# Kernel optimization log

Measured on AMD Instinct MI355X. Metric: run time of the kernel, lower is better.

Reference implementation:

```python
import jax, jax.numpy as jnp
import numpy as np

B, S, D = 8, 2048, 1024
EPS = 1e-5


def setup_inputs() -> dict:
    key = jax.random.key(0)
    ks = jax.random.split(key, 8)
    s = 1.0 / np.sqrt(D)
    return {
        "x": jax.random.normal(ks[0], (B, S, D), dtype=jnp.float32),
        "Wq": jax.random.normal(ks[1], (D, D), dtype=jnp.float32) * s,
        "bq": jnp.zeros((D,), dtype=jnp.float32),
        "Wk": jax.random.normal(ks[2], (D, D), dtype=jnp.float32) * s,
        "bk": jnp.zeros((D,), dtype=jnp.float32),
        "Wv": jax.random.normal(ks[3], (D, D), dtype=jnp.float32) * s,
        "bv": jnp.zeros((D,), dtype=jnp.float32),
        "gamma": jnp.ones((D,), dtype=jnp.float32),
        "beta": jnp.zeros((D,), dtype=jnp.float32),
    }


def reference(x, Wq, bq, Wk, bk, Wv, bv, gamma, beta):
    # Linear layers (torch convention: y = x @ W^T + b)
    Q = jnp.einsum('bsd,ed->bse', x, Wq) + bq
    K = jnp.einsum('bsd,ed->bse', x, Wk) + bk
    V = jnp.einsum('bsd,ed->bse', x, Wv) + bv
    scale = 1.0 / jnp.sqrt(jnp.asarray(D, dtype=x.dtype))
    scores = jnp.einsum('bqd,bkd->bqk', Q, K) * scale  # [B,S,S]
    attn = jax.nn.softmax(scores, axis=-1)
    out = jnp.einsum('bqk,bkd->bqd', attn, V) + x  # attention + residual
    # LayerNorm over last dim
    mu = jnp.mean(out, axis=-1, keepdims=True)
    var = jnp.var(out, axis=-1, keepdims=True)
    return (out - mu) * jax.lax.rsqrt(var + EPS) * gamma + beta
```

## Files before the change

kernel.cpp:

```cpp
#include <hip/hip_runtime.h>


typedef __bf16 bf16x8 __attribute__((ext_vector_type(8)));
typedef float f32x4 __attribute__((ext_vector_type(4)));

#define BM 128
#define BN 128
#define BK 32

enum { M_QK = 0, M_VT = 1, M_SC = 2, M_PV = 3 };

__device__ __forceinline__ unsigned short f2b(float f) {
  union { float f; unsigned int u; } v; v.f = f;
  return (unsigned short)((v.u + 0x7FFFu + ((v.u >> 16) & 1u)) >> 16);
}

__device__ __forceinline__ void gload_lds16(const void* g, void* l) {
  __builtin_amdgcn_global_load_lds(
      (const __attribute__((address_space(1))) void*)g,
      (__attribute__((address_space(3))) void*)l, 16, 0, 0);
}

template <int MODE>
__global__ __launch_bounds__(256) void gemm_bf16(
    const unsigned short* __restrict__ A, const unsigned short* __restrict__ B,
    void* __restrict__ Cv, const float* __restrict__ aux, float alpha,
    int K, int ldaE, int ldbE, int ldcE,
    size_t sA, size_t sB, size_t sC, size_t sR)
{
  const int t = threadIdx.x, l = t & 63, w = t >> 6;
  const int wm = w >> 1, wn = w & 1;
  const int bz = blockIdx.z;
  A += (size_t)bz * sA;
  B += (size_t)bz * sB;
  const int gm0 = blockIdx.y * BM, gn0 = blockIdx.x * BN;

  __shared__ __align__(16) unsigned short As[BM * BK];
  __shared__ __align__(16) unsigned short Bs[BN * BK];

  f32x4 acc[4][4];
#pragma unroll
  for (int i = 0; i < 4; ++i)
#pragma unroll
    for (int j = 0; j < 4; ++j) acc[i][j] = f32x4{0.f, 0.f, 0.f, 0.f};

  const int srow = w * 16 + (l >> 2);
  const int scolb = (l & 3) << 4;
  const int rr = l & 15;
  const int k0 = (l >> 4) << 3;

  for (int kt = 0; kt < K; kt += BK) {
    __syncthreads();
#pragma unroll
    for (int c = 0; c < 2; ++c) {
      const int r = c * 64 + srow;
      gload_lds16((const char*)(A + (size_t)(gm0 + r) * ldaE + kt) + scolb,
                  (char*)As + c * 4096 + w * 1024);
      gload_lds16((const char*)(B + (size_t)(gn0 + r) * ldbE + kt) + scolb,
                  (char*)Bs + c * 4096 + w * 1024);
    }
    __syncthreads();
    bf16x8 av[4], bv[4];
#pragma unroll
    for (int i = 0; i < 4; ++i)
      av[i] = *(const bf16x8*)&As[(wm * 64 + i * 16 + rr) * BK + k0];
#pragma unroll
    for (int j = 0; j < 4; ++j)
      bv[j] = *(const bf16x8*)&Bs[(wn * 64 + j * 16 + rr) * BK + k0];
#pragma unroll
    for (int i = 0; i < 4; ++i)
#pragma unroll
      for (int j = 0; j < 4; ++j)
        acc[i][j] = __builtin_amdgcn_mfma_f32_16x16x32_bf16(av[i], bv[j], acc[i][j], 0, 0, 0);
  }

  const int col_l = l & 15, row0_l = (l >> 4) << 2;
#pragma unroll
  for (int i = 0; i < 4; ++i) {
    const int gr = gm0 + wm * 64 + i * 16 + row0_l;
#pragma unroll
    for (int j = 0; j < 4; ++j) {
      const int gc = gn0 + wn * 64 + j * 16 + col_l;
      if constexpr (MODE == M_QK) {
        unsigned short* C = (unsigned short*)Cv;
        const float b = aux[gc];
#pragma unroll
        for (int r = 0; r < 4; ++r)
          C[(size_t)(gr + r) * ldcE + gc] = f2b(acc[i][j][r] + b);
      } else if constexpr (MODE == M_VT) {
        unsigned short* C = (unsigned short*)Cv;
        const float b = aux[gc];
        const int bat = gr >> 11, lm = gr & 2047;
        ushort4 o = make_ushort4(f2b(acc[i][j][0] + b), f2b(acc[i][j][1] + b),
                                 f2b(acc[i][j][2] + b), f2b(acc[i][j][3] + b));
        *(ushort4*)&C[(size_t)bat * sC + (size_t)gc * ldcE + lm] = o;
      } else if constexpr (MODE == M_SC) {
        float* C = (float*)Cv + (size_t)bz * sC;
        float* p = C + (size_t)gr * ldcE + gc;
#pragma unroll
        for (int r = 0; r < 4; ++r) p[(size_t)r * ldcE] = acc[i][j][r] * alpha;
      } else {
        float* C = (float*)Cv + (size_t)bz * sC;
        const float* R = aux + (size_t)bz * sR;
        float* p = C + (size_t)gr * ldcE + gc;
        const float* q = R + (size_t)gr * ldcE + gc;
#pragma unroll
        for (int r = 0; r < 4; ++r) p[(size_t)r * ldcE] = acc[i][j][r] + q[(size_t)r * ldcE];
      }
    }
  }
}

__global__ __launch_bounds__(256) void f32_to_bf16(
    const float* __restrict__ s, unsigned short* __restrict__ d)
{
  const size_t i = (size_t)blockIdx.x * 256 + threadIdx.x;
  const float4 a = ((const float4*)s)[i * 2];
  const float4 b = ((const float4*)s)[i * 2 + 1];
  ((ushort4*)d)[i * 2]     = make_ushort4(f2b(a.x), f2b(a.y), f2b(a.z), f2b(a.w));
  ((ushort4*)d)[i * 2 + 1] = make_ushort4(f2b(b.x), f2b(b.y), f2b(b.z), f2b(b.w));
}

__global__ __launch_bounds__(256) void softmax2048_bf16(float* __restrict__ S)
{
  __shared__ float redm[4];
  __shared__ float reds[4];
  const int t = threadIdx.x;
  float* p = S + (size_t)blockIdx.x * 2048;
  float4 a = *(const float4*)&p[t * 4];
  float4 b = *(const float4*)&p[t * 4 + 1024];
  float m = fmaxf(fmaxf(fmaxf(a.x, a.y), fmaxf(a.z, a.w)),
                  fmaxf(fmaxf(b.x, b.y), fmaxf(b.z, b.w)));
#pragma unroll
  for (int o = 32; o; o >>= 1) m = fmaxf(m, __shfl_xor(m, o));
  if ((t & 63) == 0) redm[t >> 6] = m;
  __syncthreads();
  m = fmaxf(fmaxf(redm[0], redm[1]), fmaxf(redm[2], redm[3]));
  a.x = __expf(a.x - m); a.y = __expf(a.y - m);
  a.z = __expf(a.z - m); a.w = __expf(a.w - m);
  b.x = __expf(b.x - m); b.y = __expf(b.y - m);
  b.z = __expf(b.z - m); b.w = __expf(b.w - m);
  float s = a.x + a.y + a.z + a.w + b.x + b.y + b.z + b.w;
#pragma unroll
  for (int o = 32; o; o >>= 1) s += __shfl_xor(s, o);
  if ((t & 63) == 0) reds[t >> 6] = s;
  __syncthreads();
  s = reds[0] + reds[1] + reds[2] + reds[3];
  const float inv = 1.0f / s;
  unsigned short* pb = (unsigned short*)p;
  *(ushort4*)&pb[t * 4] =
      make_ushort4(f2b(a.x * inv), f2b(a.y * inv), f2b(a.z * inv), f2b(a.w * inv));
  *(ushort4*)&pb[1024 + t * 4] =
      make_ushort4(f2b(b.x * inv), f2b(b.y * inv), f2b(b.z * inv), f2b(b.w * inv));
}

__global__ __launch_bounds__(64) void ln1024(
    float* __restrict__ O, const float* __restrict__ g, const float* __restrict__ be)
{
  const int l = threadIdx.x;
  float* p = O + (size_t)blockIdx.x * 1024;
  float4 v[4];
#pragma unroll
  for (int i = 0; i < 4; ++i) v[i] = *(const float4*)&p[l * 4 + i * 256];
  float s = 0.f, q = 0.f;
#pragma unroll
  for (int i = 0; i < 4; ++i) {
    s += v[i].x + v[i].y + v[i].z + v[i].w;
    q += v[i].x * v[i].x + v[i].y * v[i].y + v[i].z * v[i].z + v[i].w * v[i].w;
  }
#pragma unroll
  for (int o = 32; o; o >>= 1) { s += __shfl_xor(s, o); q += __shfl_xor(q, o); }
  const float mu = s * (1.0f / 1024.0f);
  const float var = q * (1.0f / 1024.0f) - mu * mu;
  const float rs = rsqrtf(var + 1e-5f);
#pragma unroll
  for (int i = 0; i < 4; ++i) {
    const float4 gg = *(const float4*)&g[l * 4 + i * 256];
    const float4 bb = *(const float4*)&be[l * 4 + i * 256];
    float4 o4;
    o4.x = (v[i].x - mu) * rs * gg.x + bb.x;
    o4.y = (v[i].y - mu) * rs * gg.y + bb.y;
    o4.z = (v[i].z - mu) * rs * gg.z + bb.z;
    o4.w = (v[i].w - mu) * rs * gg.w + bb.w;
    *(float4*)&p[l * 4 + i * 256] = o4;
  }
}

extern "C" void kernel_launch(void* const* d_in, const int* in_sizes, int n_in,
                              void* d_out, int out_size, void* d_ws, size_t ws_size,
                              hipStream_t stream) {
  (void)in_sizes; (void)n_in; (void)out_size; (void)ws_size;
  constexpr int Bb = 8, S = 2048, D = 1024;
  const size_t BS = (size_t)Bb * S;
  const size_t ND = BS * (size_t)D;

  const float* x     = (const float*)d_in[0];
  const float* Wq    = (const float*)d_in[1];
  const float* bq    = (const float*)d_in[2];
  const float* Wk    = (const float*)d_in[3];
  const float* bk    = (const float*)d_in[4];
  const float* Wv    = (const float*)d_in[5];
  const float* bv    = (const float*)d_in[6];
  const float* gamma = (const float*)d_in[7];
  const float* beta  = (const float*)d_in[8];
  float* out = (float*)d_out;

  unsigned short* xb = (unsigned short*)d_ws;
  unsigned short* Qb = xb + ND;
  unsigned short* Kb = Qb + ND;
  unsigned short* Vt = Kb + ND;
  float* Sbuf = (float*)(Vt + ND);
  unsigned short* Wqb = (unsigned short*)Sbuf;
  unsigned short* Wkb = Wqb + (size_t)D * D;
  unsigned short* Wvb = Wkb + (size_t)D * D;

  f32_to_bf16<<<dim3(8192), dim3(256), 0, stream>>>(x, xb);
  f32_to_bf16<<<dim3(512), dim3(256), 0, stream>>>(Wq, Wqb);
  f32_to_bf16<<<dim3(512), dim3(256), 0, stream>>>(Wk, Wkb);
  f32_to_bf16<<<dim3(512), dim3(256), 0, stream>>>(Wv, Wvb);

  const dim3 blk(256);
  const dim3 g1(D / BN, (int)(BS / BM), 1);
  gemm_bf16<M_QK><<<g1, blk, 0, stream>>>(xb, Wqb, Qb, bq, 1.f, D, D, D, D, 0, 0, 0, 0);
  gemm_bf16<M_QK><<<g1, blk, 0, stream>>>(xb, Wkb, Kb, bk, 1.f, D, D, D, D, 0, 0, 0, 0);
  gemm_bf16<M_VT><<<g1, blk, 0, stream>>>(xb, Wvb, Vt, bv, 1.f, D, D, D, S, 0, 0,
                                          (size_t)D * S, 0);
  const dim3 g2(S / BN, S / BM, Bb);
  gemm_bf16<M_SC><<<g2, blk, 0, stream>>>(Qb, Kb, Sbuf, nullptr, 0.03125f, D, D, D, S,
                                          (size_t)S * D, (size_t)S * D, (size_t)S * S, 0);
  softmax2048_bf16<<<dim3((int)BS), blk, 0, stream>>>(Sbuf);
  const dim3 g3(D / BN, S / BM, Bb);
  gemm_bf16<M_PV><<<g3, blk, 0, stream>>>(
      (const unsigned short*)Sbuf, Vt, out, x, 1.f, S, 2 * S, S, D,
      (size_t)S * 2 * S, (size_t)D * S, (size_t)S * D, (size_t)S * D);
  ln1024<<<dim3((int)BS), dim3(64), 0, stream>>>(out, gamma, beta);
}
```

Before: 613.9 us.

## Replace GEMMs with 256x256 double-buffered swizzled kernel and fuse QKV projection

```diff
diff --git a/kernel.cpp b/kernel.cpp
--- a/kernel.cpp
+++ b/kernel.cpp
@@ -4,108 +4,184 @@
 typedef __bf16 bf16x8 __attribute__((ext_vector_type(8)));
 typedef float f32x4 __attribute__((ext_vector_type(4)));
 
-#define BM 128
-#define BN 128
-#define BK 32
-
-enum { M_QK = 0, M_VT = 1, M_SC = 2, M_PV = 3 };
+enum { M_QKV = 0, M_SC = 1, M_PV = 2 };
 
 __device__ __forceinline__ unsigned short f2b(float f) {
   union { float f; unsigned int u; } v; v.f = f;
   return (unsigned short)((v.u + 0x7FFFu + ((v.u >> 16) & 1u)) >> 16);
 }
 
-__device__ __forceinline__ void gload_lds16(const void* g, void* l) {
-  __builtin_amdgcn_global_load_lds(
-      (const __attribute__((address_space(1))) void*)g,
-      (__attribute__((address_space(3))) void*)l, 16, 0, 0);
+#define GL16(gsrc, ldst)                                         \
+  __builtin_amdgcn_global_load_lds(                              \
+      (const __attribute__((address_space(1))) void*)(gsrc),     \
+      (__attribute__((address_space(3))) void*)(ldst), 16, 0, 0)
+
+__device__ __forceinline__ void stage_tile(
+    const unsigned short* Ab, const unsigned short* Bb, char* lds,
+    int b, int tau, int gm0, int gn0, int ldaE, int ldbE, int t)
+{
+  const int kc = tau << 6;
+  const int row4 = t >> 3;
+  const int c = (t & 7) << 4;
+  const int wb = (t & ~63) * 16;
+#pragma unroll
+  for (int r = 0; r < 4; ++r) {
+    const int row = r * 64 + row4;
+    const int cs = c ^ ((row & 12) << 3);
+    GL16((const char*)(Ab + (size_t)(gm0 + row) * ldaE + kc) + cs,
+         lds + b * 65536 + r * 8192 + wb);
+    __builtin_amdgcn_sched_barrier(0);
+  }
+#pragma unroll
+  for (int r = 0; r < 4; ++r) {
+    const int row = r * 64 + row4;
+    const int cs = c ^ ((row & 12) << 3);
+    GL16((const char*)(Bb + (size_t)(gn0 + row) * ldbE + kc) + cs,
+         lds + b * 65536 + 32768 + r * 8192 + wb);
+    __builtin_amdgcn_sched_barrier(0);
+  }
+}
+
+__device__ __forceinline__ bf16x8 ldsrd(const char* lds, int base, int row, int kb) {
+  int p = row * 128 + kb;
+  p ^= (p & 0x600) >> 4;
+  return *(const bf16x8*)(lds + base + p);
 }
 
 template <int MODE>
-__global__ __launch_bounds__(256) void gemm_bf16(
+__global__ __launch_bounds__(512, 2) void gemm8(
     const unsigned short* __restrict__ A, const unsigned short* __restrict__ B,
-    void* __restrict__ Cv, const float* __restrict__ aux, float alpha,
-    int K, int ldaE, int ldbE, int ldcE,
-    size_t sA, size_t sB, size_t sC, size_t sR)
-{
+    void* __restrict__ C0, void* __restrict__ C1, void* __restrict__ C2,
+    const float* __restrict__ x0, const float* __restrict__ x1,
+    const float* __restrict__ x2,
+    int K, int ldaE, int ldbE, size_t sA, size_t sB)
+{
+  extern __shared__ char lds[];
   const int t = threadIdx.x, l = t & 63, w = t >> 6;
-  const int wm = w >> 1, wn = w & 1;
   const int bz = blockIdx.z;
-  A += (size_t)bz * sA;
-  B += (size_t)bz * sB;
-  const int gm0 = blockIdx.y * BM, gn0 = blockIdx.x * BN;
-
-  __shared__ __align__(16) unsigned short As[BM * BK];
-  __shared__ __align__(16) unsigned short Bs[BN * BK];
-
-  f32x4 acc[4][4];
-#pragma unroll
-  for (int i = 0; i < 4; ++i)
-#pragma unroll
-    for (int j = 0; j < 4; ++j) acc[i][j] = f32x4{0.f, 0.f, 0.f, 0.f};
-
-  const int srow = w * 16 + (l >> 2);
-  const int scolb = (l & 3) << 4;
-  const int rr = l & 15;
-  const int k0 = (l >> 4) << 3;
-
-  for (int kt = 0; kt < K; kt += BK) {
-    __syncthreads();
-#pragma unroll
-    for (int c = 0; c < 2; ++c) {
-      const int r = c * 64 + srow;
-      gload_lds16((const char*)(A + (size_t)(gm0 + r) * ldaE + kt) + scolb,
-                  (char*)As + c * 4096 + w * 1024);
-      gload_lds16((const char*)(B + (size_t)(gn0 + r) * ldbE + kt) + scolb,
-                  (char*)Bs + c * 4096 + w * 1024);
+  const unsigned short* Ab = A + (size_t)bz * sA;
+  const unsigned short* Bb = B + (size_t)bz * sB;
+  const int gm0 = blockIdx.y * 256, gn0 = blockIdx.x * 256;
+  const int lo16 = l & 15, hi4 = l >> 4;
+  const int kb0 = hi4 * 16;
+  const int nt = K >> 6;
+
+  f32x4 acc[2][16];
+#pragma unroll
+  for (int i = 0; i < 2; ++i)
+#pragma unroll
+    for (int j = 0; j < 16; ++j) acc[i][j] = f32x4{0.f, 0.f, 0.f, 0.f};
+
+  stage_tile(Ab, Bb, lds, 0, 0, gm0, gn0, ldaE, ldbE, t);
+
+  bf16x8 af[2][2];
+  for (int tau = 0; tau < nt; ++tau) {
+    const int abase = (tau & 1) * 65536, bbase = abase + 32768;
+    const bool more = (tau + 1) < nt;
+    asm volatile("s_waitcnt vmcnt(3)" ::: "memory");
+    __builtin_amdgcn_sched_barrier(0);
+    __builtin_amdgcn_s_barrier();
+    __builtin_amdgcn_sched_barrier(0);
+    if (more)
+      stage_tile(Ab, Bb, lds, (tau & 1) ^ 1, tau + 1, gm0, gn0, ldaE, ldbE, t);
+    bf16x8 bf[4][2];
+#pragma unroll
+    for (int mf = 0; mf < 2; ++mf)
+#pragma unroll
+      for (int ks = 0; ks < 2; ++ks)
+        af[mf][ks] = ldsrd(lds, abase, w * 32 + mf * 16 + lo16, ks * 64 + kb0);
+#pragma unroll
+    for (int nf = 0; nf < 4; ++nf)
+#pragma unroll
+      for (int ks = 0; ks < 2; ++ks)
+        bf[nf][ks] = ldsrd(lds, bbase, nf * 16 + lo16, ks * 64 + kb0);
+    asm volatile("s_waitcnt lgkmcnt(0)" ::: "memory");
+    __builtin_amdgcn_sched_barrier(0);
+    __builtin_amdgcn_s_setprio(1);
+#pragma unroll
+    for (int mf = 0; mf < 2; ++mf)
+#pragma unroll
+      for (int nf = 0; nf < 4; ++nf)
+#pragma unroll
+        for (int ks = 0; ks < 2; ++ks)
+          acc[mf][nf] = __builtin_amdgcn_mfma_f32_16x16x32_bf16(
+              af[mf][ks], bf[nf][ks], acc[mf][nf], 0, 0, 0);
+    __builtin_amdgcn_s_setprio(0);
+#pragma unroll
+    for (int p = 1; p < 4; ++p) {
+      if (p == 1) {
+        if (more) asm volatile("s_waitcnt vmcnt(10)" ::: "memory");
+        else      asm volatile("s_waitcnt vmcnt(2)" ::: "memory");
+      } else if (p == 2) {
+        if (more) asm volatile("s_waitcnt vmcnt(9)" ::: "memory");
+        else      asm volatile("s_waitcnt vmcnt(1)" ::: "memory");
+      } else {
+        if (more) asm volatile("s_waitcnt vmcnt(8)" ::: "memory");
+        else      asm volatile("s_waitcnt vmcnt(0)" ::: "memory");
+      }
+      __builtin_amdgcn_sched_barrier(0);
+      __builtin_amdgcn_s_barrier();
+      __builtin_amdgcn_sched_barrier(0);
+#pragma unroll
+      for (int nf = 0; nf < 4; ++nf)
+#pragma unroll
+        for (int ks = 0; ks < 2; ++ks)
+          bf[nf][ks] = ldsrd(lds, bbase, (p * 4 + nf) * 16 + lo16, ks * 64 + kb0);
+      asm volatile("s_waitcnt lgkmcnt(0)" ::: "memory");
+      __builtin_amdgcn_sched_barrier(0);
+      __builtin_amdgcn_s_setprio(1);
+#pragma unroll
+      for (int mf = 0; mf < 2; ++mf)
+#pragma unroll
+        for (int nf = 0; nf < 4; ++nf)
+#pragma unroll
+          for (int ks = 0; ks < 2; ++ks)
+            acc[mf][p * 4 + nf] = __builtin_amdgcn_mfma_f32_16x16x32_bf16(
+                af[mf][ks], bf[nf][ks], acc[mf][p * 4 + nf], 0, 0, 0);
+      __builtin_amdgcn_s_setprio(0);
     }
-    __syncthreads();
-    bf16x8 av[4], bv[4];
-#pragma unroll
-    for (int i = 0; i < 4; ++i)
-      av[i] = *(const bf16x8*)&As[(wm * 64 + i * 16 + rr) * BK + k0];
-#pragma unroll
-    for (int j = 0; j < 4; ++j)
-      bv[j] = *(const bf16x8*)&Bs[(wn * 64 + j * 16 + rr) * BK + k0];
-#pragma unroll
-    for (int i = 0; i < 4; ++i)
-#pragma unroll
-      for (int j = 0; j < 4; ++j)
-        acc[i][j] = __builtin_amdgcn_mfma_f32_16x16x32_bf16(av[i], bv[j], acc[i][j], 0, 0, 0);
-  }
-
-  const int col_l = l & 15, row0_l = (l >> 4) << 2;
-#pragma unroll
-  for (int i = 0; i < 4; ++i) {
-    const int gr = gm0 + wm * 64 + i * 16 + row0_l;
-#pragma unroll
-    for (int j = 0; j < 4; ++j) {
-      const int gc = gn0 + wn * 64 + j * 16 + col_l;
-      if constexpr (MODE == M_QK) {
-        unsigned short* C = (unsigned short*)Cv;
-        const float b = aux[gc];
-#pragma unroll
-        for (int r = 0; r < 4; ++r)
-          C[(size_t)(gr + r) * ldcE + gc] = f2b(acc[i][j][r] + b);
-      } else if constexpr (MODE == M_VT) {
-        unsigned short* C = (unsigned short*)Cv;
-        const float b = aux[gc];
-        const int bat = gr >> 11, lm = gr & 2047;
-        ushort4 o = make_ushort4(f2b(acc[i][j][0] + b), f2b(acc[i][j][1] + b),
-                                 f2b(acc[i][j][2] + b), f2b(acc[i][j][3] + b));
-        *(ushort4*)&C[(size_t)bat * sC + (size_t)gc * ldcE + lm] = o;
+  }
+
+#pragma unroll
+  for (int mf = 0; mf < 2; ++mf) {
+    const int grow = gm0 + w * 32 + mf * 16 + hi4 * 4;
+#pragma unroll
+    for (int nf = 0; nf < 16; ++nf) {
+      const int gc = gn0 + nf * 16 + lo16;
+      if constexpr (MODE == M_QKV) {
+        if (gc < 1024) {
+          unsigned short* Q = (unsigned short*)C0;
+          const float b = x0[gc];
+#pragma unroll
+          for (int r = 0; r < 4; ++r)
+            Q[(size_t)(grow + r) * 1024 + gc] = f2b(acc[mf][nf][r] + b);
+        } else if (gc < 2048) {
+          unsigned short* Kk = (unsigned short*)C1;
+          const float b = x1[gc - 1024];
+#pragma unroll
+          for (int r = 0; r < 4; ++r)
+            Kk[(size_t)(grow + r) * 1024 + (gc - 1024)] = f2b(acc[mf][nf][r] + b);
+        } else {
+          unsigned short* Vt = (unsigned short*)C2;
+          const float b = x2[gc - 2048];
+          const int bat = grow >> 11, lm = grow & 2047;
+          ushort4 o = make_ushort4(
+              f2b(acc[mf][nf][0] + b), f2b(acc[mf][nf][1] + b),
+              f2b(acc[mf][nf][2] + b), f2b(acc[mf][nf][3] + b));
+          *(ushort4*)&Vt[(size_t)bat * 2097152 + (size_t)(gc - 2048) * 2048 + lm] = o;
+        }
       } else if constexpr (MODE == M_SC) {
-        float* C = (float*)Cv + (size_t)bz * sC;
-        float* p = C + (size_t)gr * ldcE + gc;
-#pragma unroll
-        for (int r = 0; r < 4; ++r) p[(size_t)r * ldcE] = acc[i][j][r] * alpha;
+        float* C = (float*)C0 + (size_t)bz * 4194304;
+        float* p = C + (size_t)grow * 2048 + gc;
+#pragma unroll
+        for (int r = 0; r < 4; ++r) p[(size_t)r * 2048] = acc[mf][nf][r] * 0.03125f;
       } else {
-        float* C = (float*)Cv + (size_t)bz * sC;
-        const float* R = aux + (size_t)bz * sR;
-        float* p = C + (size_t)gr * ldcE + gc;
-        const float* q = R + (size_t)gr * ldcE + gc;
-#pragma unroll
-        for (int r = 0; r < 4; ++r) p[(size_t)r * ldcE] = acc[i][j][r] + q[(size_t)r * ldcE];
+        float* C = (float*)C0 + (size_t)bz * 2097152;
+        const float* R = x0 + (size_t)bz * 2097152;
+        float* p = C + (size_t)grow * 1024 + gc;
+        const float* q = R + (size_t)grow * 1024 + gc;
+#pragma unroll
+        for (int r = 0; r < 4; ++r) p[(size_t)r * 1024] = acc[mf][nf][r] + q[(size_t)r * 1024];
       }
     }
   }
@@ -210,28 +286,28 @@
   unsigned short* Kb = Qb + ND;
   unsigned short* Vt = Kb + ND;
   float* Sbuf = (float*)(Vt + ND);
-  unsigned short* Wqb = (unsigned short*)Sbuf;
-  unsigned short* Wkb = Wqb + (size_t)D * D;
-  unsigned short* Wvb = Wkb + (size_t)D * D;
+  unsigned short* Wcat = (unsigned short*)Sbuf;
+
+  hipFuncSetAttribute((const void*)gemm8<M_QKV>,
+                      hipFuncAttributeMaxDynamicSharedMemorySize, 131072);
+  hipFuncSetAttribute((const void*)gemm8<M_SC>,
+                      hipFuncAttributeMaxDynamicSharedMemorySize, 131072);
+  hipFuncSetAttribute((const void*)gemm8<M_PV>,
+                      hipFuncAttributeMaxDynamicSharedMemorySize, 131072);
 
   f32_to_bf16<<<dim3(8192), dim3(256), 0, stream>>>(x, xb);
-  f32_to_bf16<<<dim3(512), dim3(256), 0, stream>>>(Wq, Wqb);
-  f32_to_bf16<<<dim3(512), dim3(256), 0, stream>>>(Wk, Wkb);
-  f32_to_bf16<<<dim3(512), dim3(256), 0, stream>>>(Wv, Wvb);
-
-  const dim3 blk(256);
-  const dim3 g1(D / BN, (int)(BS / BM), 1);
-  gemm_bf16<M_QK><<<g1, blk, 0, stream>>>(xb, Wqb, Qb, bq, 1.f, D, D, D, D, 0, 0, 0, 0);
-  gemm_bf16<M_QK><<<g1, blk, 0, stream>>>(xb, Wkb, Kb, bk, 1.f, D, D, D, D, 0, 0, 0, 0);
-  gemm_bf16<M_VT><<<g1, blk, 0, stream>>>(xb, Wvb, Vt, bv, 1.f, D, D, D, S, 0, 0,
-                                          (size_t)D * S, 0);
-  const dim3 g2(S / BN, S / BM, Bb);
-  gemm_bf16<M_SC><<<g2, blk, 0, stream>>>(Qb, Kb, Sbuf, nullptr, 0.03125f, D, D, D, S,
-                                          (size_t)S * D, (size_t)S * D, (size_t)S * S, 0);
-  softmax2048_bf16<<<dim3((int)BS), blk, 0, stream>>>(Sbuf);
-  const dim3 g3(D / BN, S / BM, Bb);
-  gemm_bf16<M_PV><<<g3, blk, 0, stream>>>(
-      (const unsigned short*)Sbuf, Vt, out, x, 1.f, S, 2 * S, S, D,
-      (size_t)S * 2 * S, (size_t)D * S, (size_t)S * D, (size_t)S * D);
+  f32_to_bf16<<<dim3(512), dim3(256), 0, stream>>>(Wq, Wcat);
+  f32_to_bf16<<<dim3(512), dim3(256), 0, stream>>>(Wk, Wcat + (size_t)D * D);
+  f32_to_bf16<<<dim3(512), dim3(256), 0, stream>>>(Wv, Wcat + 2 * (size_t)D * D);
+
+  gemm8<M_QKV><<<dim3(12, 64, 1), dim3(512), 131072, stream>>>(
+      xb, Wcat, Qb, Kb, Vt, bq, bk, bv, D, D, D, 0, 0);
+  gemm8<M_SC><<<dim3(8, 8, 8), dim3(512), 131072, stream>>>(
+      Qb, Kb, Sbuf, nullptr, nullptr, nullptr, nullptr, nullptr,
+      D, D, D, (size_t)S * D, (size_t)S * D);
+  softmax2048_bf16<<<dim3((int)BS), dim3(256), 0, stream>>>(Sbuf);
+  gemm8<M_PV><<<dim3(4, 8, 8), dim3(512), 131072, stream>>>(
+      (const unsigned short*)Sbuf, Vt, out, nullptr, nullptr, x, nullptr, nullptr,
+      S, 2 * S, S, (size_t)S * 2 * S, (size_t)D * S);
   ln1024<<<dim3((int)BS), dim3(64), 0, stream>>>(out, gamma, beta);
 }
```

Result: faster. 523.9 us (-14.7%).
